# Kernel tuning notes

Hardware: AMD Instinct MI355X
Metric: run time of the kernel (lower is better)

The kernel has to match this reference:

```python
import jax, jax.numpy as jnp
import numpy as np

E, T, H, I = 16, 4, 512, 1024  # expert_num, task_num, hidden_size, input_size
B = 8192


def setup_inputs() -> dict:
    key = jax.random.key(0)
    ks = jax.random.split(key, 8)
    s_i = 1.0 / np.sqrt(I)
    s_h = 1.0 / np.sqrt(H)
    return {
        "x": jax.random.normal(ks[0], (B, I), dtype=jnp.float32),
        "We": jax.random.uniform(ks[1], (E, H, I), jnp.float32, -s_i, s_i),
        "be": jax.random.uniform(ks[2], (E, H), jnp.float32, -s_i, s_i),
        "Wg": jax.random.uniform(ks[3], (T, E, I), jnp.float32, -s_i, s_i),
        "bg": jax.random.uniform(ks[4], (T, E), jnp.float32, -s_i, s_i),
        "Wf": jax.random.uniform(ks[5], (T, H), jnp.float32, -s_h, s_h),
        "bf": jax.random.uniform(ks[6], (T,), jnp.float32, -s_h, s_h),
    }


def reference(x, We, be, Wg, bg, Wf, bf):
    # expert outputs: relu(x @ We_e^T + be_e)  -> [B, E, H]
    eo = jax.nn.relu(jnp.einsum("bi,ehi->beh", x, We) + be[None])
    # gate outputs: softmax over experts        -> [B, T, E]
    g = jax.nn.softmax(jnp.einsum("bi,tei->bte", x, Wg) + bg[None], axis=-1)
    # gated combine                             -> [T, B, H]
    res = jnp.einsum("bte,beh->tbh", g, eo)
    # per-task scalar heads                     -> [T, B, 1]
    out = jnp.einsum("tbh,th->tb", res, Wf) + bf[:, None]
    return out[:, :, None]
```

## Files before the change

### kernel.cpp

```cpp
#include <hip/hip_runtime.h>
#include <hip/hip_bf16.h>
#include <stdint.h>


#define E_ 16
#define T_ 4
#define H_ 512
#define I_ 1024
#define B_ 8192
#define N_ (E_ * H_)
#define K_ I_

typedef __bf16 bf16x8 __attribute__((ext_vector_type(8)));
typedef float f32x4 __attribute__((ext_vector_type(4)));

__device__ __forceinline__ unsigned short f2bf_rne(float f) {
  unsigned int b = __float_as_uint(f);
  b += 0x7fffu + ((b >> 16) & 1u);
  return (unsigned short)(b >> 16);
}

#define N4X (B_ * K_ / 4)
#define N4W (N_ * K_ / 4)
#define N4G (64 * K_ / 4)

__global__ __launch_bounds__(256) void cvt3_kernel(const float* __restrict__ x,
                                                   const float* __restrict__ We,
                                                   const float* __restrict__ Wg,
                                                   const float* __restrict__ bfv,
                                                   unsigned short* __restrict__ xb,
                                                   unsigned short* __restrict__ wb,
                                                   unsigned short* __restrict__ wgb,
                                                   float* __restrict__ out) {
  int i = blockIdx.x * 256 + threadIdx.x;
  if (i < T_ * B_) out[i] = bfv[i >> 13];
  const float* src;
  unsigned short* dst;
  int j;
  if (i < N4X) {
    src = x; dst = xb; j = i;
  } else if (i < N4X + N4W) {
    src = We; dst = wb; j = i - N4X;
  } else if (i < N4X + N4W + N4G) {
    src = Wg; dst = wgb; j = i - (N4X + N4W);
  } else {
    return;
  }
  float4 v = reinterpret_cast<const float4*>(src)[j];
  ushort4 o;
  o.x = f2bf_rne(v.x);
  o.y = f2bf_rne(v.y);
  o.z = f2bf_rne(v.z);
  o.w = f2bf_rne(v.w);
  reinterpret_cast<ushort4*>(dst)[j] = o;
}

__device__ __forceinline__ void gld_lds16(const void* gp, void* lp) {
  __builtin_amdgcn_global_load_lds((const __attribute__((address_space(1))) void*)gp,
                                   (__attribute__((address_space(3))) void*)lp, 16, 0, 0);
}

__global__ __launch_bounds__(256) void logits_softmax_kernel(
    const unsigned short* __restrict__ A,
    const unsigned short* __restrict__ Bm,
    const float* __restrict__ bg,
    float* __restrict__ g)
{
  __shared__ struct {
    unsigned short A[128 * 32];
    unsigned short B[64 * 32];
  } st;

  const int tid = threadIdx.x;
  const int w = tid >> 6, l = tid & 63;
  const int m16 = l & 15, q = l >> 4;
  const size_t m0 = (size_t)blockIdx.x * 128;

  const int r0s = (w * 2 + 0) * 16 + (l >> 2);
  const int r1s = (w * 2 + 1) * 16 + (l >> 2);
  const int slot = l & 3;
  const int c0 = slot ^ ((r0s >> 1) & 3);
  const int c1 = slot ^ ((r1s >> 1) & 3);
  const size_t offA0 = (m0 + r0s) * K_ + c0 * 8;
  const size_t offA1 = (m0 + r1s) * K_ + c1 * 8;
  const int l0 = (w * 2 + 0) * 512;
  const int l1 = (w * 2 + 1) * 512;
  const int rBs = w * 16 + (l >> 2);
  const int cB = slot ^ ((rBs >> 1) & 3);
  const size_t offB = (size_t)rBs * K_ + cB * 8;
  const int lB = w * 512;

  const int arow = w * 32 + m16;
  const int sA = q ^ ((arow >> 1) & 3);
  const int sB = q ^ ((m16 >> 1) & 3);

  f32x4 acc[2][4] = {};

  for (int k0 = 0; k0 < K_; k0 += 32) {
    __syncthreads();
    gld_lds16(A + offA0 + k0, st.A + l0);
    gld_lds16(A + offA1 + k0, st.A + l1);
    gld_lds16(Bm + offB + k0, st.B + lB);
    __syncthreads();
    bf16x8 af[2], bfr[4];
#pragma unroll
    for (int i = 0; i < 2; ++i)
      af[i] = *reinterpret_cast<const bf16x8*>(st.A + (arow + i * 16) * 32 + sA * 8);
#pragma unroll
    for (int j = 0; j < 4; ++j)
      bfr[j] = *reinterpret_cast<const bf16x8*>(st.B + (j * 16 + m16) * 32 + sB * 8);
#pragma unroll
    for (int i = 0; i < 2; ++i)
#pragma unroll
      for (int j = 0; j < 4; ++j)
        acc[i][j] = __builtin_amdgcn_mfma_f32_16x16x32_bf16(af[i], bfr[j], acc[i][j], 0, 0, 0);
  }

  float bgv[4];
#pragma unroll
  for (int j = 0; j < 4; ++j) bgv[j] = bg[j * 16 + m16];

#pragma unroll
  for (int i = 0; i < 2; ++i) {
    float lg[4][4];
#pragma unroll
    for (int j = 0; j < 4; ++j)
#pragma unroll
      for (int r = 0; r < 4; ++r) lg[r][j] = acc[i][j][r] + bgv[j];
#pragma unroll
    for (int r = 0; r < 4; ++r) {
#pragma unroll
      for (int j = 0; j < 4; ++j) {
        float m = lg[r][j];
#pragma unroll
        for (int mask = 1; mask < 16; mask <<= 1) m = fmaxf(m, __shfl_xor(m, mask, 64));
        float ex = __expf(lg[r][j] - m);
        float s = ex;
#pragma unroll
        for (int mask = 1; mask < 16; mask <<= 1) s += __shfl_xor(s, mask, 64);
        size_t b = m0 + w * 32 + i * 16 + q * 4 + r;
        g[b * 64 + j * 16 + m16] = ex / s;
      }
    }
  }
}


extern __shared__ char smem[];

#define BARRIER()                          \
  do {                                     \
    asm volatile("" ::: "memory");         \
    __builtin_amdgcn_s_barrier();          \
    asm volatile("" ::: "memory");         \
  } while (0)
#define VMW(n) asm volatile("s_waitcnt vmcnt(" #n ")" ::: "memory")

#define STAGE_A(d, h, kk)                                                              \
  do {                                                                                 \
    gld_lds16(A + baseAg + (h)*131072 + (kk), smem + (d)*65536 + (h)*16384 + ldsW);    \
    gld_lds16(A + baseAg + (h)*131072 + 8192 + (kk),                                   \
              smem + (d)*65536 + (h)*16384 + ldsW + 1024);                             \
  } while (0)
#define STAGE_B(d, h, kk)                                                              \
  do {                                                                                 \
    gld_lds16(Bm + baseBg + (h)*131072 + (kk),                                         \
              smem + (d)*65536 + 32768 + (h)*16384 + ldsW);                            \
    gld_lds16(Bm + baseBg + (h)*131072 + 8192 + (kk),                                  \
              smem + (d)*65536 + 32768 + (h)*16384 + ldsW + 1024);                     \
  } while (0)

#define LDA4(d, ib)                                                                       \
  do {                                                                                    \
    _Pragma("unroll") for (int i2 = 0; i2 < 4; ++i2) {                                    \
      af[i2][0] = *reinterpret_cast<const bf16x8*>(smem + (d)*65536 + baseA_rd +          \
                                                   ((ib) + i2) * 2048 + slK0);            \
      af[i2][1] = *reinterpret_cast<const bf16x8*>(smem + (d)*65536 + baseA_rd +          \
                                                   ((ib) + i2) * 2048 + slK1);            \
    }                                                                                     \
  } while (0)
#define LDB2(d, jb)                                                                       \
  do {                                                                                    \
    _Pragma("unroll") for (int j2 = 0; j2 < 2; ++j2) {                                    \
      bfr[(jb) + j2][0] = *reinterpret_cast<const bf16x8*>(smem + (d)*65536 + baseB_rd +  \
                                                           ((jb) + j2) * 2048 + slK0);    \
      bfr[(jb) + j2][1] = *reinterpret_cast<const bf16x8*>(smem + (d)*65536 + baseB_rd +  \
                                                           ((jb) + j2) * 2048 + slK1);    \
    }                                                                                     \
  } while (0)

#define MFMAQ(ib, jb)                                                                     \
  do {                                                                                    \
    __builtin_amdgcn_s_setprio(1);                                                        \
    _Pragma("unroll") for (int i2 = 0; i2 < 4; ++i2)                                      \
        _Pragma("unroll") for (int j2 = 0; j2 < 2; ++j2) {                                \
      acc[(ib) + i2][(jb) + j2] = __builtin_amdgcn_mfma_f32_16x16x32_bf16(                \
          af[i2][0], bfr[(jb) + j2][0], acc[(ib) + i2][(jb) + j2], 0, 0, 0);              \
      acc[(ib) + i2][(jb) + j2] = __builtin_amdgcn_mfma_f32_16x16x32_bf16(                \
          af[i2][1], bfr[(jb) + j2][1], acc[(ib) + i2][(jb) + j2], 0, 0, 0);              \
    }                                                                                     \
    __builtin_amdgcn_s_setprio(0);                                                        \
  } while (0)

__global__ __launch_bounds__(512, 2) void moe_main_kernel(
    const unsigned short* __restrict__ A,
    const unsigned short* __restrict__ Bm,
    const float* __restrict__ be,
    const float* __restrict__ Wf,
    const float* __restrict__ g,
    float* __restrict__ out)
{
  const int tid = threadIdx.x;
  const int w = tid >> 6, l = tid & 63;
  const int wm = w >> 2, wn = w & 3;
  const int m16 = l & 15, q = l >> 4;
  const int mb = blockIdx.x, nb = blockIdx.y;
  const size_t m0 = (size_t)mb * 256, n0 = (size_t)nb * 256;

  const size_t baseAg = (m0 + w * 16 + (l >> 3)) * K_ + (size_t)(((l & 7) ^ (l >> 3)) * 8);
  const size_t baseBg = (n0 + w * 16 + (l >> 3)) * K_ + (size_t)(((l & 7) ^ (l >> 3)) * 8);
  const int ldsW = w * 2048;

  const int slK0 = ((q) ^ (m16 & 7)) * 16;
  const int slK1 = ((4 + q) ^ (m16 & 7)) * 16;
  const int baseA_rd = (wm * 128 + m16) * 128;
  const int baseB_rd = 32768 + (wn * 64 + m16) * 128;

  f32x4 acc[8][4] = {};
  bf16x8 af[4][2], bfr[4][2];

  STAGE_A(0, 0, 0);
  STAGE_A(0, 1, 0);
  STAGE_B(0, 0, 0);
  STAGE_B(0, 1, 0);
  STAGE_B(1, 0, 64);
  STAGE_B(1, 1, 64);
  VMW(4);
  BARRIER();

#pragma unroll 1
  for (int n = 0; n < 7; ++n) {
    const int kA1 = (2 * n + 1) * 64;
    const int kN2 = (2 * n + 2) * 64;
    const int kB3 = (2 * n + 3) * 64;
    LDA4(0, 0); LDB2(0, 0); STAGE_A(1, 0, kA1);
    BARRIER(); MFMAQ(0, 0); BARRIER();
    LDB2(0, 2); STAGE_A(1, 1, kA1);
    BARRIER(); MFMAQ(0, 2); BARRIER();
    LDA4(0, 4); STAGE_B(0, 0, kN2);
    BARRIER(); MFMAQ(4, 2); BARRIER();
    STAGE_B(0, 1, kN2); VMW(4);
    BARRIER(); MFMAQ(4, 0); BARRIER();
    LDA4(1, 0); LDB2(1, 0); STAGE_A(0, 0, kN2);
    BARRIER(); MFMAQ(0, 0); BARRIER();
    LDB2(1, 2); STAGE_A(0, 1, kN2);
    BARRIER(); MFMAQ(0, 2); BARRIER();
    LDA4(1, 4); STAGE_B(1, 0, kB3);
    BARRIER(); MFMAQ(4, 2); BARRIER();
    STAGE_B(1, 1, kB3); VMW(4);
    BARRIER(); MFMAQ(4, 0); BARRIER();
  }

  LDA4(0, 0); LDB2(0, 0); STAGE_A(1, 0, 15 * 64);
  BARRIER(); MFMAQ(0, 0); BARRIER();
  LDB2(0, 2); STAGE_A(1, 1, 15 * 64);
  BARRIER(); MFMAQ(0, 2); BARRIER();
  LDA4(0, 4);
  BARRIER(); MFMAQ(4, 2); BARRIER();
  VMW(0);
  BARRIER(); MFMAQ(4, 0); BARRIER();
  LDA4(1, 0); LDB2(1, 0);
  BARRIER(); MFMAQ(0, 0); BARRIER();
  LDB2(1, 2);
  BARRIER(); MFMAQ(0, 2); BARRIER();
  LDA4(1, 4);
  BARRIER(); MFMAQ(4, 2); BARRIER();
  MFMAQ(4, 0);

  float* allsums = (float*)smem;

  const int hb = (int)(n0 & 511);
  const int e_idx = (int)(n0 >> 9);

  float wfv[4][4];
#pragma unroll
  for (int t = 0; t < 4; ++t)
#pragma unroll
    for (int j = 0; j < 4; ++j)
      wfv[t][j] = Wf[t * H_ + hb + wn * 64 + j * 16 + m16];
  float bias[4];
#pragma unroll
  for (int j = 0; j < 4; ++j) bias[j] = be[n0 + wn * 64 + j * 16 + m16];

  const int b0s = m16 & 1, b1s = (m16 >> 1) & 1, b2s = (m16 >> 2) & 1, b3s = (m16 >> 3) & 1;
#pragma unroll
  for (int i = 0; i < 8; ++i) {
    float eo[4][4];
#pragma unroll
    for (int j = 0; j < 4; ++j)
#pragma unroll
      for (int r = 0; r < 4; ++r) eo[j][r] = fmaxf(acc[i][j][r] + bias[j], 0.f);
    float p[16];
#pragma unroll
    for (int r = 0; r < 4; ++r)
#pragma unroll
      for (int t = 0; t < 4; ++t) {
        float v = 0.f;
#pragma unroll
        for (int j = 0; j < 4; ++j) v += eo[j][r] * wfv[t][j];
        p[r * 4 + t] = v;
      }
    float q8[8];
#pragma unroll
    for (int m = 0; m < 8; ++m) {
      float sent = b0s ? p[2 * m] : p[2 * m + 1];
      float recv = __shfl_xor(sent, 1, 64);
      q8[m] = (b0s ? p[2 * m + 1] : p[2 * m]) + recv;
    }
    float q4[4];
#pragma unroll
    for (int u = 0; u < 4; ++u) {
      float sent = b1s ? q8[2 * u] : q8[2 * u + 1];
      float recv = __shfl_xor(sent, 2, 64);
      q4[u] = (b1s ? q8[2 * u + 1] : q8[2 * u]) + recv;
    }
    float q2[2];
#pragma unroll
    for (int u = 0; u < 2; ++u) {
      float sent = b2s ? q4[2 * u] : q4[2 * u + 1];
      float recv = __shfl_xor(sent, 4, 64);
      q2[u] = (b2s ? q4[2 * u + 1] : q4[2 * u]) + recv;
    }
    float sent = b3s ? q2[0] : q2[1];
    float recv = __shfl_xor(sent, 8, 64);
    float v = (b3s ? q2[1] : q2[0]) + recv;

    int row = wm * 128 + i * 16 + q * 4 + (m16 >> 2);
    allsums[wn * 1024 + row * 4 + (m16 & 3)] = v;
  }
  __syncthreads();

  {
    float2 s = *reinterpret_cast<float2*>(&allsums[0 * 1024 + tid * 2]);
    float2 x1 = *reinterpret_cast<float2*>(&allsums[1 * 1024 + tid * 2]);
    float2 x2 = *reinterpret_cast<float2*>(&allsums[2 * 1024 + tid * 2]);
    float2 x3 = *reinterpret_cast<float2*>(&allsums[3 * 1024 + tid * 2]);
    s.x += x1.x + x2.x + x3.x;
    s.y += x1.y + x2.y + x3.y;
#pragma unroll
    for (int oi = 0; oi < 2; ++oi) {
      int o = tid * 2 + oi;
      int row = o >> 2, t = o & 3;
      float sv = oi ? s.y : s.x;
      size_t b = m0 + row;
      float gv = g[b * 64 + t * 16 + e_idx];
      atomicAdd(&out[(size_t)t * B_ + b], gv * sv);
    }
  }
}

extern "C" void kernel_launch(void* const* d_in, const int* in_sizes, int n_in,
                              void* d_out, int out_size, void* d_ws, size_t ws_size,
                              hipStream_t stream) {
  const float* x = (const float*)d_in[0];
  const float* We = (const float*)d_in[1];
  const float* be = (const float*)d_in[2];
  const float* Wg = (const float*)d_in[3];
  const float* bg = (const float*)d_in[4];
  const float* Wf = (const float*)d_in[5];
  const float* bf = (const float*)d_in[6];
  float* out = (float*)d_out;

  unsigned short* xb = (unsigned short*)d_ws;
  unsigned short* wb = xb + (size_t)B_ * K_;
  unsigned short* wgb = wb + (size_t)N_ * K_;
  float* g = (float*)(wgb + (size_t)64 * K_);

  hipFuncSetAttribute((const void*)moe_main_kernel,
                      hipFuncAttributeMaxDynamicSharedMemorySize, 131072);

  cvt3_kernel<<<(N4X + N4W + N4G + 255) / 256, 256, 0, stream>>>(x, We, Wg, bf, xb, wb, wgb, out);
  logits_softmax_kernel<<<B_ / 128, 256, 0, stream>>>(xb, wgb, bg, g);
  dim3 grid(B_ / 256, N_ / 256);
  moe_main_kernel<<<grid, 512, 131072, stream>>>(xb, wb, be, Wf, g, out);
}
```

Baseline: 250.3 us.

## Process four N-tiles per block with cross-tile prefetch and fused per-expert reduction

Each block now loops over four consecutive 256-wide N tiles covering two experts. It keeps the same M tile, prefetches the next tile's A and B into shared memory during the tail of the current tile, and accumulates the per-expert partial sums in registers. This cuts the number of atomic adds to the output by a factor of four and amortizes block launch and epilogue setup. The cost is a grid of 32x8 = 256 blocks instead of 1024, which may reduce occupancy balance and latency hiding across CUs. A is also re-streamed for each tile.

```diff
diff --git a/kernel.cpp b/kernel.cpp
--- a/kernel.cpp
+++ b/kernel.cpp
@@ -155,6 +155,7 @@
     asm volatile("" ::: "memory");         \
   } while (0)
 #define VMW(n) asm volatile("s_waitcnt vmcnt(" #n ")" ::: "memory")
+#define LGKM0() asm volatile("s_waitcnt lgkmcnt(0)" ::: "memory")
 
 #define STAGE_A(d, h, kk)                                                              \
   do {                                                                                 \
@@ -162,11 +163,11 @@
     gld_lds16(A + baseAg + (h)*131072 + 8192 + (kk),                                   \
               smem + (d)*65536 + (h)*16384 + ldsW + 1024);                             \
   } while (0)
-#define STAGE_B(d, h, kk)                                                              \
+#define STAGE_B(base, d, h, kk)                                                        \
   do {                                                                                 \
-    gld_lds16(Bm + baseBg + (h)*131072 + (kk),                                         \
+    gld_lds16(Bm + (base) + (h)*131072 + (kk),                                         \
               smem + (d)*65536 + 32768 + (h)*16384 + ldsW);                            \
-    gld_lds16(Bm + baseBg + (h)*131072 + 8192 + (kk),                                  \
+    gld_lds16(Bm + (base) + (h)*131072 + 8192 + (kk),                                  \
               smem + (d)*65536 + 32768 + (h)*16384 + ldsW + 1024);                     \
   } while (0)
 
@@ -214,11 +215,12 @@
   const int w = tid >> 6, l = tid & 63;
   const int wm = w >> 2, wn = w & 3;
   const int m16 = l & 15, q = l >> 4;
-  const int mb = blockIdx.x, nb = blockIdx.y;
-  const size_t m0 = (size_t)mb * 256, n0 = (size_t)nb * 256;
+  const int mb = blockIdx.x, nbg = blockIdx.y;
+  const size_t m0 = (size_t)mb * 256;
 
   const size_t baseAg = (m0 + w * 16 + (l >> 3)) * K_ + (size_t)(((l & 7) ^ (l >> 3)) * 8);
-  const size_t baseBg = (n0 + w * 16 + (l >> 3)) * K_ + (size_t)(((l & 7) ^ (l >> 3)) * 8);
+  const size_t baseBg0 =
+      ((size_t)nbg * 4 * 256 + w * 16 + (l >> 3)) * K_ + (size_t)(((l & 7) ^ (l >> 3)) * 8);
   const int ldsW = w * 2048;
 
   const int slK0 = ((q) ^ (m16 & 7)) * 16;
@@ -226,137 +228,165 @@
   const int baseA_rd = (wm * 128 + m16) * 128;
   const int baseB_rd = 32768 + (wn * 64 + m16) * 128;
 
-  f32x4 acc[8][4] = {};
+  const int row_o = tid >> 1;
+  const int t0 = 2 * (tid & 1);
+  const size_t b_o = m0 + row_o;
+  const int e0 = nbg * 2;
+  const float gvA0 = g[b_o * 64 + t0 * 16 + e0];
+  const float gvA1 = g[b_o * 64 + (t0 + 1) * 16 + e0];
+  const float gvB0 = g[b_o * 64 + t0 * 16 + e0 + 1];
+  const float gvB1 = g[b_o * 64 + (t0 + 1) * 16 + e0 + 1];
+
+  f32x4 acc[8][4];
   bf16x8 af[4][2], bfr[4][2];
+  float2 accE0 = {0.f, 0.f}, accE1 = {0.f, 0.f};
 
   STAGE_A(0, 0, 0);
   STAGE_A(0, 1, 0);
-  STAGE_B(0, 0, 0);
-  STAGE_B(0, 1, 0);
-  STAGE_B(1, 0, 64);
-  STAGE_B(1, 1, 64);
+  STAGE_B(baseBg0, 0, 0, 0);
+  STAGE_B(baseBg0, 0, 1, 0);
+  STAGE_B(baseBg0, 1, 0, 64);
+  STAGE_B(baseBg0, 1, 1, 64);
   VMW(4);
   BARRIER();
 
 #pragma unroll 1
-  for (int n = 0; n < 7; ++n) {
-    const int kA1 = (2 * n + 1) * 64;
-    const int kN2 = (2 * n + 2) * 64;
-    const int kB3 = (2 * n + 3) * 64;
-    LDA4(0, 0); LDB2(0, 0); STAGE_A(1, 0, kA1);
+  for (int it = 0; it < 4; ++it) {
+    const size_t bB = baseBg0 + (size_t)it * (256 * K_);
+    const size_t bBn = bB + (size_t)(256 * K_);
+
+#pragma unroll
+    for (int i = 0; i < 8; ++i)
+#pragma unroll
+      for (int j = 0; j < 4; ++j) acc[i][j] = (f32x4){0.f, 0.f, 0.f, 0.f};
+
+#pragma unroll 1
+    for (int n = 0; n < 7; ++n) {
+      const int kA1 = (2 * n + 1) * 64;
+      const int kN2 = (2 * n + 2) * 64;
+      const int kB3 = (2 * n + 3) * 64;
+      LDA4(0, 0); LDB2(0, 0); STAGE_A(1, 0, kA1);
+      BARRIER(); MFMAQ(0, 0); BARRIER();
+      LDB2(0, 2); STAGE_A(1, 1, kA1);
+      BARRIER(); MFMAQ(0, 2); BARRIER();
+      LDA4(0, 4); STAGE_B(bB, 0, 0, kN2);
+      BARRIER(); MFMAQ(4, 2); BARRIER();
+      STAGE_B(bB, 0, 1, kN2); VMW(4);
+      BARRIER(); MFMAQ(4, 0); BARRIER();
+      LDA4(1, 0); LDB2(1, 0); STAGE_A(0, 0, kN2);
+      BARRIER(); MFMAQ(0, 0); BARRIER();
+      LDB2(1, 2); STAGE_A(0, 1, kN2);
+      BARRIER(); MFMAQ(0, 2); BARRIER();
+      LDA4(1, 4); STAGE_B(bB, 1, 0, kB3);
+      BARRIER(); MFMAQ(4, 2); BARRIER();
+      STAGE_B(bB, 1, 1, kB3); VMW(4);
+      BARRIER(); MFMAQ(4, 0); BARRIER();
+    }
+
+    const bool pf = (it < 3);
+    LDA4(0, 0); LDB2(0, 0); STAGE_A(1, 0, 15 * 64);
     BARRIER(); MFMAQ(0, 0); BARRIER();
-    LDB2(0, 2); STAGE_A(1, 1, kA1);
+    LDB2(0, 2); STAGE_A(1, 1, 15 * 64);
     BARRIER(); MFMAQ(0, 2); BARRIER();
-    LDA4(0, 4); STAGE_B(0, 0, kN2);
+    LDA4(0, 4);
     BARRIER(); MFMAQ(4, 2); BARRIER();
-    STAGE_B(0, 1, kN2); VMW(4);
+    VMW(0);
     BARRIER(); MFMAQ(4, 0); BARRIER();
-    LDA4(1, 0); LDB2(1, 0); STAGE_A(0, 0, kN2);
+    LDA4(1, 0); LDB2(1, 0);
+    if (pf) STAGE_A(0, 0, 0);
     BARRIER(); MFMAQ(0, 0); BARRIER();
-    LDB2(1, 2); STAGE_A(0, 1, kN2);
+    LDB2(1, 2);
+    if (pf) STAGE_A(0, 1, 0);
     BARRIER(); MFMAQ(0, 2); BARRIER();
-    LDA4(1, 4); STAGE_B(1, 0, kB3);
+    LDA4(1, 4);
+    if (pf) STAGE_B(bBn, 0, 0, 0);
     BARRIER(); MFMAQ(4, 2); BARRIER();
-    STAGE_B(1, 1, kB3); VMW(4);
-    BARRIER(); MFMAQ(4, 0); BARRIER();
-  }
-
-  LDA4(0, 0); LDB2(0, 0); STAGE_A(1, 0, 15 * 64);
-  BARRIER(); MFMAQ(0, 0); BARRIER();
-  LDB2(0, 2); STAGE_A(1, 1, 15 * 64);
-  BARRIER(); MFMAQ(0, 2); BARRIER();
-  LDA4(0, 4);
-  BARRIER(); MFMAQ(4, 2); BARRIER();
-  VMW(0);
-  BARRIER(); MFMAQ(4, 0); BARRIER();
-  LDA4(1, 0); LDB2(1, 0);
-  BARRIER(); MFMAQ(0, 0); BARRIER();
-  LDB2(1, 2);
-  BARRIER(); MFMAQ(0, 2); BARRIER();
-  LDA4(1, 4);
-  BARRIER(); MFMAQ(4, 2); BARRIER();
-  MFMAQ(4, 0);
-
-  float* allsums = (float*)smem;
-
-  const int hb = (int)(n0 & 511);
-  const int e_idx = (int)(n0 >> 9);
-
-  float wfv[4][4];
-#pragma unroll
-  for (int t = 0; t < 4; ++t)
-#pragma unroll
-    for (int j = 0; j < 4; ++j)
-      wfv[t][j] = Wf[t * H_ + hb + wn * 64 + j * 16 + m16];
-  float bias[4];
-#pragma unroll
-  for (int j = 0; j < 4; ++j) bias[j] = be[n0 + wn * 64 + j * 16 + m16];
-
-  const int b0s = m16 & 1, b1s = (m16 >> 1) & 1, b2s = (m16 >> 2) & 1, b3s = (m16 >> 3) & 1;
-#pragma unroll
-  for (int i = 0; i < 8; ++i) {
-    float eo[4][4];
-#pragma unroll
-    for (int j = 0; j < 4; ++j)
-#pragma unroll
-      for (int r = 0; r < 4; ++r) eo[j][r] = fmaxf(acc[i][j][r] + bias[j], 0.f);
-    float p[16];
-#pragma unroll
-    for (int r = 0; r < 4; ++r)
-#pragma unroll
-      for (int t = 0; t < 4; ++t) {
-        float v = 0.f;
-#pragma unroll
-        for (int j = 0; j < 4; ++j) v += eo[j][r] * wfv[t][j];
-        p[r * 4 + t] = v;
+    if (pf) { STAGE_B(bBn, 0, 1, 0); STAGE_B(bBn, 1, 0, 64); STAGE_B(bBn, 1, 1, 64); }
+    MFMAQ(4, 0);
+
+    float* allsums = (float*)(smem + 65536);
+
+    const size_t n0v = ((size_t)nbg * 4 + it) * 256;
+    const int hb = (it & 1) * 256;
+
+    float wfv[4][4];
+#pragma unroll
+    for (int t = 0; t < 4; ++t)
+#pragma unroll
+      for (int j = 0; j < 4; ++j)
+        wfv[t][j] = Wf[t * H_ + hb + wn * 64 + j * 16 + m16];
+    float bias[4];
+#pragma unroll
+    for (int j = 0; j < 4; ++j) bias[j] = be[n0v + wn * 64 + j * 16 + m16];
+
+    const int b0s = m16 & 1, b1s = (m16 >> 1) & 1, b2s = (m16 >> 2) & 1, b3s = (m16 >> 3) & 1;
+#pragma unroll
+    for (int i = 0; i < 8; ++i) {
+      float eo[4][4];
+#pragma unroll
+      for (int j = 0; j < 4; ++j)
+#pragma unroll
+        for (int r = 0; r < 4; ++r) eo[j][r] = fmaxf(acc[i][j][r] + bias[j], 0.f);
+      float p[16];
+#pragma unroll
+      for (int r = 0; r < 4; ++r)
+#pragma unroll
+        for (int t = 0; t < 4; ++t) {
+          float v = 0.f;
+#pragma unroll
+          for (int j = 0; j < 4; ++j) v += eo[j][r] * wfv[t][j];
+          p[r * 4 + t] = v;
+        }
+      float q8[8];
+#pragma unroll
+      for (int m = 0; m < 8; ++m) {
+        float sent = b0s ? p[2 * m] : p[2 * m + 1];
+        float recv = __shfl_xor(sent, 1, 64);
+        q8[m] = (b0s ? p[2 * m + 1] : p[2 * m]) + recv;
       }
-    float q8[8];
-#pragma unroll
-    for (int m = 0; m < 8; ++m) {
-      float sent = b0s ? p[2 * m] : p[2 * m + 1];
-      float recv = __shfl_xor(sent, 1, 64);
-      q8[m] = (b0s ? p[2 * m + 1] : p[2 * m]) + recv;
+      float q4[4];
+#pragma unroll
+      for (int u = 0; u < 4; ++u) {
+        float sent = b1s ? q8[2 * u] : q8[2 * u + 1];
+        float recv = __shfl_xor(sent, 2, 64);
+        q4[u] = (b1s ? q8[2 * u + 1] : q8[2 * u]) + recv;
+      }
+      float q2[2];
+#pragma unroll
+      for (int u = 0; u < 2; ++u) {
+        float sent = b2s ? q4[2 * u] : q4[2 * u + 1];
+        float recv = __shfl_xor(sent, 4, 64);
+        q2[u] = (b2s ? q4[2 * u + 1] : q4[2 * u]) + recv;
+      }
+      float sent = b3s ? q2[0] : q2[1];
+      float recv = __shfl_xor(sent, 8, 64);
+      float v = (b3s ? q2[1] : q2[0]) + recv;
+
+      int row = wm * 128 + i * 16 + q * 4 + (m16 >> 2);
+      allsums[wn * 1024 + row * 4 + (m16 & 3)] = v;
     }
-    float q4[4];
-#pragma unroll
-    for (int u = 0; u < 4; ++u) {
-      float sent = b1s ? q8[2 * u] : q8[2 * u + 1];
-      float recv = __shfl_xor(sent, 2, 64);
-      q4[u] = (b1s ? q8[2 * u + 1] : q8[2 * u]) + recv;
+    LGKM0();
+    BARRIER();
+
+    float2 s0 = *reinterpret_cast<float2*>(&allsums[0 * 1024 + tid * 2]);
+    float2 s1 = *reinterpret_cast<float2*>(&allsums[1 * 1024 + tid * 2]);
+    float2 s2 = *reinterpret_cast<float2*>(&allsums[2 * 1024 + tid * 2]);
+    float2 s3 = *reinterpret_cast<float2*>(&allsums[3 * 1024 + tid * 2]);
+    const float sx = s0.x + s1.x + s2.x + s3.x;
+    const float sy = s0.y + s1.y + s2.y + s3.y;
+    if (pf) {
+      VMW(4);
+      BARRIER();
     }
-    float q2[2];
-#pragma unroll
-    for (int u = 0; u < 2; ++u) {
-      float sent = b2s ? q4[2 * u] : q4[2 * u + 1];
-      float recv = __shfl_xor(sent, 4, 64);
-      q2[u] = (b2s ? q4[2 * u + 1] : q4[2 * u]) + recv;
-    }
-    float sent = b3s ? q2[0] : q2[1];
-    float recv = __shfl_xor(sent, 8, 64);
-    float v = (b3s ? q2[1] : q2[0]) + recv;
-
-    int row = wm * 128 + i * 16 + q * 4 + (m16 >> 2);
-    allsums[wn * 1024 + row * 4 + (m16 & 3)] = v;
-  }
-  __syncthreads();
-
-  {
-    float2 s = *reinterpret_cast<float2*>(&allsums[0 * 1024 + tid * 2]);
-    float2 x1 = *reinterpret_cast<float2*>(&allsums[1 * 1024 + tid * 2]);
-    float2 x2 = *reinterpret_cast<float2*>(&allsums[2 * 1024 + tid * 2]);
-    float2 x3 = *reinterpret_cast<float2*>(&allsums[3 * 1024 + tid * 2]);
-    s.x += x1.x + x2.x + x3.x;
-    s.y += x1.y + x2.y + x3.y;
-#pragma unroll
-    for (int oi = 0; oi < 2; ++oi) {
-      int o = tid * 2 + oi;
-      int row = o >> 2, t = o & 3;
-      float sv = oi ? s.y : s.x;
-      size_t b = m0 + row;
-      float gv = g[b * 64 + t * 16 + e_idx];
-      atomicAdd(&out[(size_t)t * B_ + b], gv * sv);
+    if (it < 2) {
+      accE0.x += sx; accE0.y += sy;
+    } else {
+      accE1.x += sx; accE1.y += sy;
     }
   }
+
+  atomicAdd(&out[(size_t)t0 * B_ + b_o], gvA0 * accE0.x + gvB0 * accE1.x);
+  atomicAdd(&out[(size_t)(t0 + 1) * B_ + b_o], gvA1 * accE0.y + gvB1 * accE1.y);
 }
 
 extern "C" void kernel_launch(void* const* d_in, const int* in_sizes, int n_in,
@@ -381,6 +411,6 @@
 
   cvt3_kernel<<<(N4X + N4W + N4G + 255) / 256, 256, 0, stream>>>(x, We, Wg, bf, xb, wb, wgb, out);
   logits_softmax_kernel<<<B_ / 128, 256, 0, stream>>>(xb, wgb, bg, g);
-  dim3 grid(B_ / 256, N_ / 256);
+  dim3 grid(B_ / 256, N_ / (256 * 4));
   moe_main_kernel<<<grid, 512, 131072, stream>>>(xb, wb, be, Wf, g, out);
 }
```

Result: slower. 256.6 us (+2.5%).

## Replace ping-pong K64 pipeline with 4-stage K32 ring buffer

Applied to the files above, without the earlier changes.

Restructures the GEMM main loop from a two-buffer, K=64 schedule with eight barrier-separated quarter MFMA phases into a four-slot ring of K=32 tiles. Each iteration issues loads three tiles ahead and then computes one full tile, with a single barrier per step. The global-to-LDS addressing and swizzle are reworked for 64-byte rows. This cuts barrier count and deepens prefetch, but gives each step less MFMA work to hide LDS reads and raises the number of steps.

```diff
diff --git a/kernel.cpp b/kernel.cpp
--- a/kernel.cpp
+++ b/kernel.cpp
@@ -155,51 +155,32 @@
     asm volatile("" ::: "memory");         \
   } while (0)
 #define VMW(n) asm volatile("s_waitcnt vmcnt(" #n ")" ::: "memory")
-
-#define STAGE_A(d, h, kk)                                                              \
-  do {                                                                                 \
-    gld_lds16(A + baseAg + (h)*131072 + (kk), smem + (d)*65536 + (h)*16384 + ldsW);    \
-    gld_lds16(A + baseAg + (h)*131072 + 8192 + (kk),                                   \
-              smem + (d)*65536 + (h)*16384 + ldsW + 1024);                             \
+#define LGKM0() asm volatile("s_waitcnt lgkmcnt(0)" ::: "memory")
+
+#define STAGE4(t_)                                                             \
+  do {                                                                         \
+    const int bb_ = ((t_) & 3) * 32768;                                        \
+    const int ko_ = (t_) * 32;                                                 \
+    gld_lds16(A + baseAg + ko_, smem + bb_ + ldsW);                            \
+    gld_lds16(A + baseAg + 16 * K_ + ko_, smem + bb_ + ldsW + 1024);           \
+    gld_lds16(Bm + baseBg + ko_, smem + bb_ + 16384 + ldsW);                   \
+    gld_lds16(Bm + baseBg + 16 * K_ + ko_, smem + bb_ + 16384 + ldsW + 1024);  \
   } while (0)
-#define STAGE_B(d, h, kk)                                                              \
-  do {                                                                                 \
-    gld_lds16(Bm + baseBg + (h)*131072 + (kk),                                         \
-              smem + (d)*65536 + 32768 + (h)*16384 + ldsW);                            \
-    gld_lds16(Bm + baseBg + (h)*131072 + 8192 + (kk),                                  \
-              smem + (d)*65536 + 32768 + (h)*16384 + ldsW + 1024);                     \
-  } while (0)
-
-#define LDA4(d, ib)                                                                       \
-  do {                                                                                    \
-    _Pragma("unroll") for (int i2 = 0; i2 < 4; ++i2) {                                    \
-      af[i2][0] = *reinterpret_cast<const bf16x8*>(smem + (d)*65536 + baseA_rd +          \
-                                                   ((ib) + i2) * 2048 + slK0);            \
-      af[i2][1] = *reinterpret_cast<const bf16x8*>(smem + (d)*65536 + baseA_rd +          \
-                                                   ((ib) + i2) * 2048 + slK1);            \
-    }                                                                                     \
-  } while (0)
-#define LDB2(d, jb)                                                                       \
-  do {                                                                                    \
-    _Pragma("unroll") for (int j2 = 0; j2 < 2; ++j2) {                                    \
-      bfr[(jb) + j2][0] = *reinterpret_cast<const bf16x8*>(smem + (d)*65536 + baseB_rd +  \
-                                                           ((jb) + j2) * 2048 + slK0);    \
-      bfr[(jb) + j2][1] = *reinterpret_cast<const bf16x8*>(smem + (d)*65536 + baseB_rd +  \
-                                                           ((jb) + j2) * 2048 + slK1);    \
-    }                                                                                     \
-  } while (0)
-
-#define MFMAQ(ib, jb)                                                                     \
-  do {                                                                                    \
-    __builtin_amdgcn_s_setprio(1);                                                        \
-    _Pragma("unroll") for (int i2 = 0; i2 < 4; ++i2)                                      \
-        _Pragma("unroll") for (int j2 = 0; j2 < 2; ++j2) {                                \
-      acc[(ib) + i2][(jb) + j2] = __builtin_amdgcn_mfma_f32_16x16x32_bf16(                \
-          af[i2][0], bfr[(jb) + j2][0], acc[(ib) + i2][(jb) + j2], 0, 0, 0);              \
-      acc[(ib) + i2][(jb) + j2] = __builtin_amdgcn_mfma_f32_16x16x32_bf16(                \
-          af[i2][1], bfr[(jb) + j2][1], acc[(ib) + i2][(jb) + j2], 0, 0, 0);              \
-    }                                                                                     \
-    __builtin_amdgcn_s_setprio(0);                                                        \
+
+#define COMPUTE(t_)                                                                     \
+  do {                                                                                  \
+    const int bb_ = ((t_) & 3) * 32768;                                                 \
+    bf16x8 af[8], bfr[4];                                                               \
+    _Pragma("unroll") for (int i = 0; i < 8; ++i) af[i] =                               \
+        *reinterpret_cast<const bf16x8*>(smem + bb_ + baseA_rd + i * 1024 + sl16);      \
+    _Pragma("unroll") for (int j = 0; j < 4; ++j) bfr[j] =                              \
+        *reinterpret_cast<const bf16x8*>(smem + bb_ + 16384 + baseB_rd + j * 1024 + sl16); \
+    __builtin_amdgcn_s_setprio(1);                                                      \
+    _Pragma("unroll") for (int i = 0; i < 8; ++i)                                       \
+        _Pragma("unroll") for (int j = 0; j < 4; ++j)                                   \
+            acc[i][j] = __builtin_amdgcn_mfma_f32_16x16x32_bf16(af[i], bfr[j],          \
+                                                                acc[i][j], 0, 0, 0);   \
+    __builtin_amdgcn_s_setprio(0);                                                      \
   } while (0)
 
 __global__ __launch_bounds__(512, 2) void moe_main_kernel(
@@ -217,65 +198,43 @@
   const int mb = blockIdx.x, nb = blockIdx.y;
   const size_t m0 = (size_t)mb * 256, n0 = (size_t)nb * 256;
 
-  const size_t baseAg = (m0 + w * 16 + (l >> 3)) * K_ + (size_t)(((l & 7) ^ (l >> 3)) * 8);
-  const size_t baseBg = (n0 + w * 16 + (l >> 3)) * K_ + (size_t)(((l & 7) ^ (l >> 3)) * 8);
+  const int c8 = (((l & 3) ^ ((l >> 3) & 3)) * 8);
+  const size_t baseAg = (m0 + w * 32 + (l >> 2)) * K_ + c8;
+  const size_t baseBg = (n0 + w * 32 + (l >> 2)) * K_ + c8;
   const int ldsW = w * 2048;
 
-  const int slK0 = ((q) ^ (m16 & 7)) * 16;
-  const int slK1 = ((4 + q) ^ (m16 & 7)) * 16;
-  const int baseA_rd = (wm * 128 + m16) * 128;
-  const int baseB_rd = 32768 + (wn * 64 + m16) * 128;
+  const int sl16 = (q ^ ((m16 >> 1) & 3)) * 16;
+  const int baseA_rd = (wm * 128 + m16) * 64;
+  const int baseB_rd = (wn * 64 + m16) * 64;
 
   f32x4 acc[8][4] = {};
-  bf16x8 af[4][2], bfr[4][2];
-
-  STAGE_A(0, 0, 0);
-  STAGE_A(0, 1, 0);
-  STAGE_B(0, 0, 0);
-  STAGE_B(0, 1, 0);
-  STAGE_B(1, 0, 64);
-  STAGE_B(1, 1, 64);
+
+  STAGE4(0);
+  STAGE4(1);
+  STAGE4(2);
+
+#pragma unroll 1
+  for (int t = 0; t < 29; ++t) {
+    VMW(8);
+    BARRIER();
+    STAGE4(t + 3);
+    COMPUTE(t);
+    LGKM0();
+  }
+  VMW(8);
+  BARRIER();
+  COMPUTE(29);
+  LGKM0();
   VMW(4);
   BARRIER();
-
-#pragma unroll 1
-  for (int n = 0; n < 7; ++n) {
-    const int kA1 = (2 * n + 1) * 64;
-    const int kN2 = (2 * n + 2) * 64;
-    const int kB3 = (2 * n + 3) * 64;
-    LDA4(0, 0); LDB2(0, 0); STAGE_A(1, 0, kA1);
-    BARRIER(); MFMAQ(0, 0); BARRIER();
-    LDB2(0, 2); STAGE_A(1, 1, kA1);
-    BARRIER(); MFMAQ(0, 2); BARRIER();
-    LDA4(0, 4); STAGE_B(0, 0, kN2);
-    BARRIER(); MFMAQ(4, 2); BARRIER();
-    STAGE_B(0, 1, kN2); VMW(4);
-    BARRIER(); MFMAQ(4, 0); BARRIER();
-    LDA4(1, 0); LDB2(1, 0); STAGE_A(0, 0, kN2);
-    BARRIER(); MFMAQ(0, 0); BARRIER();
-    LDB2(1, 2); STAGE_A(0, 1, kN2);
-    BARRIER(); MFMAQ(0, 2); BARRIER();
-    LDA4(1, 4); STAGE_B(1, 0, kB3);
-    BARRIER(); MFMAQ(4, 2); BARRIER();
-    STAGE_B(1, 1, kB3); VMW(4);
-    BARRIER(); MFMAQ(4, 0); BARRIER();
-  }
-
-  LDA4(0, 0); LDB2(0, 0); STAGE_A(1, 0, 15 * 64);
-  BARRIER(); MFMAQ(0, 0); BARRIER();
-  LDB2(0, 2); STAGE_A(1, 1, 15 * 64);
-  BARRIER(); MFMAQ(0, 2); BARRIER();
-  LDA4(0, 4);
-  BARRIER(); MFMAQ(4, 2); BARRIER();
+  COMPUTE(30);
+  LGKM0();
   VMW(0);
-  BARRIER(); MFMAQ(4, 0); BARRIER();
-  LDA4(1, 0); LDB2(1, 0);
-  BARRIER(); MFMAQ(0, 0); BARRIER();
-  LDB2(1, 2);
-  BARRIER(); MFMAQ(0, 2); BARRIER();
-  LDA4(1, 4);
-  BARRIER(); MFMAQ(4, 2); BARRIER();
-  MFMAQ(4, 0);
+  BARRIER();
+  COMPUTE(31);
+  LGKM0();
+
+  __syncthreads();
 
   float* allsums = (float*)smem;
 
```

After: 259.4 us. +3.6%, slower.
